# Performance work log

Measured on AMD Instinct MI355X. Metric: run time of the kernel, lower is better.

Reference implementation:

```python
import jax, jax.numpy as jnp
import numpy as np

N = 20000          # nodes
E = 320000         # edges (before self loops)
IN_DIM = 64
HID = 128
HEADS = 4
LAYERS = 3
GRAPHS = 64
NEG_SLOPE = 0.2
LN_EPS = 1e-5


def setup_inputs() -> dict:
    key = jax.random.key(0)
    ks = jax.random.split(key, 12)
    x = jax.random.normal(ks[0], (N, IN_DIM), dtype=jnp.float32)
    edge_index = jax.random.randint(ks[1], (2, E), 0, N, dtype=jnp.int64)
    batch = jnp.sort(jax.random.randint(ks[2], (N,), 0, GRAPHS, dtype=jnp.int64))
    s = 0.05
    W_in = jax.random.normal(ks[3], (IN_DIM, HID), dtype=jnp.float32) * s
    b_in = jnp.zeros((HID,), dtype=jnp.float32)
    Ws = jax.random.normal(ks[4], (LAYERS, HID, HEADS * HID), dtype=jnp.float32) * s
    att_src = jax.random.normal(ks[5], (LAYERS, HEADS, HID), dtype=jnp.float32) * s
    att_dst = jax.random.normal(ks[6], (LAYERS, HEADS, HID), dtype=jnp.float32) * s
    conv_b = jnp.zeros((LAYERS, HID), dtype=jnp.float32)
    ln_g = jnp.ones((LAYERS, HID), dtype=jnp.float32)
    ln_b = jnp.zeros((LAYERS, HID), dtype=jnp.float32)
    return {"x": x, "edge_index": edge_index, "batch": batch,
            "W_in": W_in, "b_in": b_in, "Ws": Ws, "att_src": att_src,
            "att_dst": att_dst, "conv_b": conv_b, "ln_g": ln_g, "ln_b": ln_b}


def _gat_layer(x, src, dst, W, a_src, a_dst, bias):
    # x: [N, HID] -> h: [N, HEADS, HID]
    h = (x @ W).reshape(N, HEADS, HID)
    alpha_s = jnp.einsum('nhc,hc->nh', h, a_src)   # [N, H]
    alpha_d = jnp.einsum('nhc,hc->nh', h, a_dst)   # [N, H]
    e = jax.nn.leaky_relu(alpha_s[src] + alpha_d[dst], NEG_SLOPE)  # [E', H]
    # segment softmax over destination node (every node has a self loop)
    m = jax.ops.segment_max(e, dst, num_segments=N)
    e = jnp.exp(e - m[dst])
    denom = jax.ops.segment_sum(e, dst, num_segments=N)
    a = e / (denom[dst] + 1e-16)                    # [E', H]
    msg = h[src] * a[:, :, None]                    # [E', H, HID]
    out = jax.ops.segment_sum(msg, dst, num_segments=N)  # [N, H, HID]
    return out.mean(axis=1) + bias                  # concat=False -> head mean


def _layer_norm(x, g, b):
    mu = x.mean(axis=-1, keepdims=True)
    var = ((x - mu) ** 2).mean(axis=-1, keepdims=True)
    return (x - mu) * jax.lax.rsqrt(var + LN_EPS) * g + b


def reference(x, edge_index, batch, W_in, b_in, Ws, att_src, att_dst, conv_b, ln_g, ln_b):
    # add self loops (PyG GATConv default)
    loops = jnp.arange(N, dtype=edge_index.dtype)
    src = jnp.concatenate([edge_index[0], loops])
    dst = jnp.concatenate([edge_index[1], loops])

    h = x @ W_in + b_in
    for l in range(LAYERS):
        conv = _gat_layer(h, src, dst, Ws[l], att_src[l], att_dst[l], conv_b[l])
        h = _layer_norm(jax.nn.relu(conv) + h, ln_g[l], ln_b[l])

    # global mean pool over graphs
    sums = jax.ops.segment_sum(h, batch, num_segments=GRAPHS)
    cnt = jax.ops.segment_sum(jnp.ones((N,), dtype=h.dtype), batch, num_segments=GRAPHS)
    return sums / jnp.maximum(cnt, 1.0)[:, None]
```

## Files before the change

kernel.cpp:

```cpp
#include <hip/hip_runtime.h>
#include <hip/hip_bf16.h>
#include <math.h>

#define N_NODES 20000
#define N_EDGES 320000
#define IN_DIM 64
#define HID 128
#define HEADS 4
#define LAYERS 3
#define GRAPHS 64
#define TOT_E (N_EDGES + N_NODES)
#define NEG_SLOPE 0.2f
#define LN_EPS 1e-5f
#define MAXD 96
#define OB 132

typedef __attribute__((ext_vector_type(8))) short short8v;
typedef __attribute__((ext_vector_type(4))) float f32x4;
typedef __attribute__((ext_vector_type(2))) float f32x2;

__device__ __forceinline__ float blo(unsigned int u) { return __uint_as_float(u << 16); }
__device__ __forceinline__ float bhi(unsigned int u) { return __uint_as_float(u & 0xffff0000u); }


__global__ void zero_kernel(int* __restrict__ cursor) {
    int i = blockIdx.x * blockDim.x + threadIdx.x;
    if (i < N_NODES) cursor[i] = 0;
}

__global__ void fill_slots(const int* __restrict__ ei, int* __restrict__ cursor,
                           int* __restrict__ slots) {
    int e = blockIdx.x * blockDim.x + threadIdx.x;
    if (e >= TOT_E) return;
    int src, dst;
    if (e < N_EDGES) { src = ei[e]; dst = ei[N_EDGES + e]; }
    else { src = e - N_EDGES; dst = src; }
    int pos = atomicAdd(&cursor[dst], 1);
    if (pos < MAXD) slots[dst * MAXD + pos] = src;
}


#define NV (LAYERS * 128 * 512)
#define NWIN (HID * IN_DIM)
#define NX (N_NODES * IN_DIM)
#define NU (LAYERS * HEADS * HID)

__global__ void pack_all(const float* __restrict__ Ws, const float* __restrict__ W_in,
                         const float* __restrict__ x, const float* __restrict__ att_src,
                         const float* __restrict__ att_dst,
                         __hip_bfloat16* __restrict__ Vt, __hip_bfloat16* __restrict__ Wt_in,
                         __hip_bfloat16* __restrict__ xb,
                         float* __restrict__ u_s, float* __restrict__ u_d) {
    int i = blockIdx.x * blockDim.x + threadIdx.x;
    if (i < NV) {
        int l = i / 65536;
        int r = i % 65536;
        int c = r / 512, hk = r % 512;
        int hh = hk >> 7, k = hk & 127;
        Vt[i] = __float2bfloat16(0.25f * Ws[(size_t)l * 65536 + k * 512 + hh * 128 + c]);
    } else if (i < NV + NWIN) {
        int r = i - NV;
        int n = r / 64, k = r % 64;
        Wt_in[r] = __float2bfloat16(W_in[k * 128 + n]);
    } else if (i < NV + NWIN + NX) {
        int r = i - NV - NWIN;
        xb[r] = __float2bfloat16(x[r]);
    } else if (i < NV + NWIN + NX + NU) {
        int t = i - NV - NWIN - NX;
        int l = t / 512;
        int r = t % 512;
        int hh = r / 128, k = r % 128;
        const float* wrow = Ws + (size_t)l * 65536 + k * 512 + hh * 128;
        const float* as = att_src + l * 512 + hh * 128;
        const float* ad = att_dst + l * 512 + hh * 128;
        float ss = 0.f, sd = 0.f;
        for (int c = 0; c < 128; ++c) {
            float w = wrow[c];
            ss = fmaf(w, as[c], ss);
            sd = fmaf(w, ad[c], sd);
        }
        u_s[t] = ss; u_d[t] = sd;
    }
}


__global__ __launch_bounds__(256) void gemm_in(
    const __hip_bfloat16* __restrict__ Ax,
    const __hip_bfloat16* __restrict__ Bt,
    const float* __restrict__ bias,
    const float* __restrict__ u_s0, const float* __restrict__ u_d0,
    float* __restrict__ h, unsigned char* __restrict__ h8,
    float* __restrict__ a_s, float* __restrict__ a_d) {
    __shared__ __hip_bfloat16 As[64 * 64];
    const int M_ = N_NODES;
    int tid = threadIdx.x;
    int lane = tid & 63, w = tid >> 6;
    int lr = lane & 15, lg = lane >> 4;
    int row0 = blockIdx.x * 64;
#pragma unroll
    for (int it = 0; it < 2; ++it) {
        int chunk = it * 256 + tid;
        int row = chunk >> 3, c8 = chunk & 7;
        int sc = c8 ^ (row & 7);
        int gr = row0 + row; if (gr >= M_) gr = M_ - 1;
        const __hip_bfloat16* src = Ax + (size_t)gr * 64 + sc * 8;
        __builtin_amdgcn_global_load_lds(
            (const void __attribute__((address_space(1)))*)src,
            (void __attribute__((address_space(3)))*)(As + chunk * 8), 16, 0, 0);
    }
    __syncthreads();

    f32x4 acc[8] = {};
    int rl = w * 16 + lr;
#pragma unroll
    for (int ks = 0; ks < 2; ++ks) {
        int kc = ks * 4 + lg;
        short8v a = *(const short8v*)&As[(rl * 8 + (kc ^ (rl & 7))) * 8];
#pragma unroll
        for (int nf = 0; nf < 8; ++nf) {
            short8v b = *(const short8v*)&Bt[(size_t)(nf * 16 + lr) * 64 + ks * 32 + lg * 8];
            acc[nf] = __builtin_amdgcn_mfma_f32_16x16x32_bf16(a, b, acc[nf], 0, 0, 0);
        }
    }

    float cb[8], us[4][8], ud[4][8];
#pragma unroll
    for (int nf = 0; nf < 8; ++nf) cb[nf] = bias[nf * 16 + lr];
#pragma unroll
    for (int hh = 0; hh < 4; ++hh)
#pragma unroll
        for (int nf = 0; nf < 8; ++nf) {
            us[hh][nf] = u_s0[hh * 128 + nf * 16 + lr];
            ud[hh][nf] = u_d0[hh * 128 + nf * 16 + lr];
        }

#pragma unroll
    for (int j = 0; j < 4; ++j) {
        int r = row0 + w * 16 + lg * 4 + j;
        if (r >= M_) continue;
        float vals[8];
#pragma unroll
        for (int nf = 0; nf < 8; ++nf) {
            float v = acc[nf][j] + cb[nf];
            vals[nf] = v;
            h[(size_t)r * HID + nf * 16 + lr] = v;
            int d = __builtin_amdgcn_cvt_pk_fp8_f32(v, v, 0, false);
            h8[(size_t)r * HID + nf * 16 + lr] = (unsigned char)(d & 0xff);
        }
#pragma unroll
        for (int hh = 0; hh < 4; ++hh) {
            float ps = 0.f, pd = 0.f;
#pragma unroll
            for (int nf = 0; nf < 8; ++nf) {
                ps = fmaf(vals[nf], us[hh][nf], ps);
                pd = fmaf(vals[nf], ud[hh][nf], pd);
            }
            ps += __shfl_xor(ps, 1); pd += __shfl_xor(pd, 1);
            ps += __shfl_xor(ps, 2); pd += __shfl_xor(pd, 2);
            ps += __shfl_xor(ps, 4); pd += __shfl_xor(pd, 4);
            ps += __shfl_xor(ps, 8); pd += __shfl_xor(pd, 8);
            if (lr == 0) { a_s[r * 4 + hh] = ps; a_d[r * 4 + hh] = pd; }
        }
    }
}


__global__ __launch_bounds__(256) void layer_fused(
    const int* __restrict__ deg_arr, const int* __restrict__ slots,
    const unsigned char* __restrict__ h8i, const float* __restrict__ a_si,
    const float* __restrict__ a_di,
    const __hip_bfloat16* __restrict__ Vt,
    const float* __restrict__ conv_b, const float* __restrict__ ln_g,
    const float* __restrict__ ln_b,
    const float* __restrict__ u_sn, const float* __restrict__ u_dn,
    float* __restrict__ h, unsigned char* __restrict__ h8o,
    float* __restrict__ a_so, float* __restrict__ a_do, int last) {
    __shared__ __attribute__((aligned(16))) __hip_bfloat16 aggLds[16 * 512];
    __shared__ __attribute__((aligned(16))) char uMem[16 * OB * 4];
    float* outb = (float*)uMem;
    float (*eLds)[MAXD * 4] = (float(*)[MAXD * 4])uMem;
    int (*sLds)[MAXD] = (int(*)[MAXD])(uMem + 4 * MAXD * 4 * 4);

    int tid = threadIdx.x;
    int lane = tid & 63, wv = tid >> 6;
    int row0 = blockIdx.x * 16;
    int hh = lane >> 4;
    int j  = lane & 15;
    const unsigned char* hbase = h8i + j * 8;

    for (int t = 0; t < 4; ++t) {
        int row = wv * 4 + t;
        int n = row0 + row;
        int deg = deg_arr[n]; if (deg > MAXD) deg = MAXD;
        int beg = n * MAXD;

        int ja = lane >> 2, ha = lane & 3;
        float adh = a_di[n * 4 + ha];
        float mx = -3.4e38f;
        for (int c = 0; c < deg; c += 16) {
            int idx = c + ja;
            float e = -3.4e38f;
            if (idx < deg) {
                int s = slots[beg + idx];
                if (ha == 0) sLds[wv][idx] = s;
                e = a_si[s * 4 + ha] + adh;
                e = (e > 0.f) ? e : NEG_SLOPE * e;
            }
            eLds[wv][idx * 4 + ha] = e;
            mx = fmaxf(mx, e);
        }
        mx = fmaxf(mx, __shfl_xor(mx, 4));
        mx = fmaxf(mx, __shfl_xor(mx, 8));
        mx = fmaxf(mx, __shfl_xor(mx, 16));
        mx = fmaxf(mx, __shfl_xor(mx, 32));
        float dsum = 0.f;
        for (int c = 0; c < deg; c += 16) {
            int idx = c + ja;
            if (idx < deg) {
                float p = __expf(eLds[wv][idx * 4 + ha] - mx);
                eLds[wv][idx * 4 + ha] = p;
                dsum += p;
            }
        }
        dsum += __shfl_xor(dsum, 4);
        dsum += __shfl_xor(dsum, 8);
        dsum += __shfl_xor(dsum, 16);
        dsum += __shfl_xor(dsum, 32);
        float dh = __shfl(dsum, hh);
        float inv_own = 1.f / (dh + 1e-16f);

        float acc[8] = {0.f, 0.f, 0.f, 0.f, 0.f, 0.f, 0.f, 0.f};
        int i = 0;
        for (; i + 3 < deg; i += 4) {
            int ss[4]; float pp[4]; uint2 uu[4];
#pragma unroll
            for (int k = 0; k < 4; ++k) {
                ss[k] = sLds[wv][i + k];
                pp[k] = eLds[wv][(i + k) * 4 + hh];
            }
#pragma unroll
            for (int k = 0; k < 4; ++k)
                uu[k] = *(const uint2*)(hbase + (size_t)ss[k] * HID);
#pragma unroll
            for (int k = 0; k < 4; ++k) {
                f32x2 a01 = __builtin_amdgcn_cvt_pk_f32_fp8(uu[k].x, false);
                f32x2 a23 = __builtin_amdgcn_cvt_pk_f32_fp8(uu[k].x, true);
                f32x2 a45 = __builtin_amdgcn_cvt_pk_f32_fp8(uu[k].y, false);
                f32x2 a67 = __builtin_amdgcn_cvt_pk_f32_fp8(uu[k].y, true);
                acc[0] = fmaf(pp[k], a01[0], acc[0]);
                acc[1] = fmaf(pp[k], a01[1], acc[1]);
                acc[2] = fmaf(pp[k], a23[0], acc[2]);
                acc[3] = fmaf(pp[k], a23[1], acc[3]);
                acc[4] = fmaf(pp[k], a45[0], acc[4]);
                acc[5] = fmaf(pp[k], a45[1], acc[5]);
                acc[6] = fmaf(pp[k], a67[0], acc[6]);
                acc[7] = fmaf(pp[k], a67[1], acc[7]);
            }
        }
        for (; i < deg; ++i) {
            int s0 = sLds[wv][i];
            float p0 = eLds[wv][i * 4 + hh];
            uint2 u0 = *(const uint2*)(hbase + (size_t)s0 * HID);
            f32x2 a01 = __builtin_amdgcn_cvt_pk_f32_fp8(u0.x, false);
            f32x2 a23 = __builtin_amdgcn_cvt_pk_f32_fp8(u0.x, true);
            f32x2 a45 = __builtin_amdgcn_cvt_pk_f32_fp8(u0.y, false);
            f32x2 a67 = __builtin_amdgcn_cvt_pk_f32_fp8(u0.y, true);
            acc[0] = fmaf(p0, a01[0], acc[0]);
            acc[1] = fmaf(p0, a01[1], acc[1]);
            acc[2] = fmaf(p0, a23[0], acc[2]);
            acc[3] = fmaf(p0, a23[1], acc[3]);
            acc[4] = fmaf(p0, a45[0], acc[4]);
            acc[5] = fmaf(p0, a45[1], acc[5]);
            acc[6] = fmaf(p0, a67[0], acc[6]);
            acc[7] = fmaf(p0, a67[1], acc[7]);
        }

        __hip_bfloat162 q[4];
#pragma unroll
        for (int k = 0; k < 4; ++k) {
            q[k].x = __float2bfloat16(acc[2 * k] * inv_own);
            q[k].y = __float2bfloat16(acc[2 * k + 1] * inv_own);
        }
        *(uint4*)&aggLds[row * 512 + (16 * hh + (j ^ row)) * 8] = *(uint4*)q;
    }
    __syncthreads();

    int lr = lane & 15, lg = lane >> 4;
    f32x4 macc[2] = {};
    const __hip_bfloat16* Bb0 = Vt + (size_t)(wv * 32 + lr) * 512;
    const __hip_bfloat16* Bb1 = Vt + (size_t)(wv * 32 + 16 + lr) * 512;
#pragma unroll
    for (int ks = 0; ks < 16; ++ks) {
        int kc = ks * 4 + lg;
        int pos = (kc & ~15) | ((kc & 15) ^ lr);
        short8v a = *(const short8v*)&aggLds[lr * 512 + pos * 8];
        int ko = ks * 32 + lg * 8;
        short8v b0 = *(const short8v*)(Bb0 + ko);
        short8v b1 = *(const short8v*)(Bb1 + ko);
        macc[0] = __builtin_amdgcn_mfma_f32_16x16x32_bf16(a, b0, macc[0], 0, 0, 0);
        macc[1] = __builtin_amdgcn_mfma_f32_16x16x32_bf16(a, b1, macc[1], 0, 0, 0);
    }
    __syncthreads();
#pragma unroll
    for (int nf = 0; nf < 2; ++nf)
#pragma unroll
        for (int jj = 0; jj < 4; ++jj)
            outb[(lg * 4 + jj) * OB + wv * 32 + nf * 16 + lr] = macc[nf][jj];
    __syncthreads();

    int row = tid >> 4, q = tid & 15;
    int r = row0 + row;
    int c0 = q * 8;
    float v[8];
#pragma unroll
    for (int c = 0; c < 8; ++c) v[c] = outb[row * OB + c0 + c];

    float4 cb0 = *(const float4*)&conv_b[c0];
    float4 cb1 = *(const float4*)&conv_b[c0 + 4];
    float cb[8] = {cb0.x, cb0.y, cb0.z, cb0.w, cb1.x, cb1.y, cb1.z, cb1.w};
    float4 h0 = *(const float4*)&h[(size_t)r * HID + c0];
    float4 h1 = *(const float4*)&h[(size_t)r * HID + c0 + 4];
    float hr[8] = {h0.x, h0.y, h0.z, h0.w, h1.x, h1.y, h1.z, h1.w};
    float s1 = 0.f;
#pragma unroll
    for (int c = 0; c < 8; ++c) {
        v[c] = fmaxf(v[c] + cb[c], 0.f) + hr[c];
        s1 += v[c];
    }
    s1 += __shfl_xor(s1, 1); s1 += __shfl_xor(s1, 2);
    s1 += __shfl_xor(s1, 4); s1 += __shfl_xor(s1, 8);
    float mu = s1 * (1.f / HID);
    float s2 = 0.f;
#pragma unroll
    for (int c = 0; c < 8; ++c) {
        v[c] -= mu;
        s2 += v[c] * v[c];
    }
    s2 += __shfl_xor(s2, 1); s2 += __shfl_xor(s2, 2);
    s2 += __shfl_xor(s2, 4); s2 += __shfl_xor(s2, 8);
    float rstd = rsqrtf(s2 * (1.f / HID) + LN_EPS);
    float4 g0 = *(const float4*)&ln_g[c0];
    float4 g1 = *(const float4*)&ln_g[c0 + 4];
    float4 b0 = *(const float4*)&ln_b[c0];
    float4 b1 = *(const float4*)&ln_b[c0 + 4];
    float gg[8] = {g0.x, g0.y, g0.z, g0.w, g1.x, g1.y, g1.z, g1.w};
    float bb[8] = {b0.x, b0.y, b0.z, b0.w, b1.x, b1.y, b1.z, b1.w};
    float o[8];
#pragma unroll
    for (int c = 0; c < 8; ++c) o[c] = v[c] * rstd * gg[c] + bb[c];

    *(float4*)&h[(size_t)r * HID + c0] = make_float4(o[0], o[1], o[2], o[3]);
    *(float4*)&h[(size_t)r * HID + c0 + 4] = make_float4(o[4], o[5], o[6], o[7]);
    int d0 = 0, d1 = 0;
    d0 = __builtin_amdgcn_cvt_pk_fp8_f32(o[0], o[1], d0, false);
    d0 = __builtin_amdgcn_cvt_pk_fp8_f32(o[2], o[3], d0, true);
    d1 = __builtin_amdgcn_cvt_pk_fp8_f32(o[4], o[5], d1, false);
    d1 = __builtin_amdgcn_cvt_pk_fp8_f32(o[6], o[7], d1, true);
    *(uint2*)&h8o[(size_t)r * HID + c0] = make_uint2((unsigned)d0, (unsigned)d1);

    if (!last) {
#pragma unroll
        for (int ah = 0; ah < 4; ++ah) {
            float4 usa = *(const float4*)&u_sn[ah * 128 + c0];
            float4 usb = *(const float4*)&u_sn[ah * 128 + c0 + 4];
            float4 uda = *(const float4*)&u_dn[ah * 128 + c0];
            float4 udb = *(const float4*)&u_dn[ah * 128 + c0 + 4];
            float ps = o[0] * usa.x + o[1] * usa.y + o[2] * usa.z + o[3] * usa.w +
                       o[4] * usb.x + o[5] * usb.y + o[6] * usb.z + o[7] * usb.w;
            float pd = o[0] * uda.x + o[1] * uda.y + o[2] * uda.z + o[3] * uda.w +
                       o[4] * udb.x + o[5] * udb.y + o[6] * udb.z + o[7] * udb.w;
            ps += __shfl_xor(ps, 1); pd += __shfl_xor(pd, 1);
            ps += __shfl_xor(ps, 2); pd += __shfl_xor(pd, 2);
            ps += __shfl_xor(ps, 4); pd += __shfl_xor(pd, 4);
            ps += __shfl_xor(ps, 8); pd += __shfl_xor(pd, 8);
            if (q == 0) { a_so[r * 4 + ah] = ps; a_do[r * 4 + ah] = pd; }
        }
    }
}


__global__ __launch_bounds__(128) void pool2_kernel(
    const float* __restrict__ h, const int* __restrict__ batch,
    float* __restrict__ out) {
    int g = blockIdx.x;
    int c = threadIdx.x;
    __shared__ int sLo, sHi;
    if (c == 0) {
        int lo = 0, hi = N_NODES;
        while (lo < hi) { int m = (lo + hi) >> 1; if (batch[m] < g) lo = m + 1; else hi = m; }
        sLo = lo;
        hi = N_NODES;
        while (lo < hi) { int m = (lo + hi) >> 1; if (batch[m] < g + 1) lo = m + 1; else hi = m; }
        sHi = lo;
    }
    __syncthreads();
    int lo = sLo, hi = sHi;
    float s0 = 0.f, s1 = 0.f, s2 = 0.f, s3 = 0.f;
    int n = lo;
    for (; n + 3 < hi; n += 4) {
        s0 += h[(size_t)n * HID + c];
        s1 += h[(size_t)(n + 1) * HID + c];
        s2 += h[(size_t)(n + 2) * HID + c];
        s3 += h[(size_t)(n + 3) * HID + c];
    }
    for (; n < hi; ++n) s0 += h[(size_t)n * HID + c];
    float s = (s0 + s1) + (s2 + s3);
    int cnt = hi - lo; if (cnt < 1) cnt = 1;
    out[g * HID + c] = s / (float)cnt;
}


extern "C" void kernel_launch(void* const* d_in, const int* in_sizes, int n_in,
                              void* d_out, int out_size, void* d_ws, size_t ws_size,
                              hipStream_t stream) {
    const float* x      = (const float*)d_in[0];
    const int*   ei     = (const int*)d_in[1];
    const int*   batch  = (const int*)d_in[2];
    const float* W_in   = (const float*)d_in[3];
    const float* b_in   = (const float*)d_in[4];
    const float* Ws     = (const float*)d_in[5];
    const float* att_src= (const float*)d_in[6];
    const float* att_dst= (const float*)d_in[7];
    const float* conv_b = (const float*)d_in[8];
    const float* ln_g   = (const float*)d_in[9];
    const float* ln_b   = (const float*)d_in[10];
    float* out = (float*)d_out;

    char* ws = (char*)d_ws;
    size_t off = 0;
    auto alloc = [&](size_t bytes) -> void* {
        void* p = ws + off;
        off = (off + bytes + 255) & ~(size_t)255;
        return p;
    };
    float* h            = (float*)alloc((size_t)N_NODES * HID * 4);
    unsigned char* h8a  = (unsigned char*)alloc((size_t)N_NODES * HID);
    unsigned char* h8b  = (unsigned char*)alloc((size_t)N_NODES * HID);
    __hip_bfloat16* Vt  = (__hip_bfloat16*)alloc((size_t)NV * 2);
    __hip_bfloat16* Wti = (__hip_bfloat16*)alloc((size_t)NWIN * 2);
    __hip_bfloat16* xb  = (__hip_bfloat16*)alloc((size_t)NX * 2);
    float* u_s    = (float*)alloc((size_t)NU * 4);
    float* u_d    = (float*)alloc((size_t)NU * 4);
    float* a_sa   = (float*)alloc((size_t)N_NODES * HEADS * 4);
    float* a_sb   = (float*)alloc((size_t)N_NODES * HEADS * 4);
    float* a_da   = (float*)alloc((size_t)N_NODES * HEADS * 4);
    float* a_db   = (float*)alloc((size_t)N_NODES * HEADS * 4);
    int* cursor   = (int*)alloc(N_NODES * 4);
    int* slots    = (int*)alloc((size_t)N_NODES * MAXD * 4);

    zero_kernel<<<(N_NODES + 255) / 256, 256, 0, stream>>>(cursor);
    fill_slots<<<(TOT_E + 255) / 256, 256, 0, stream>>>(ei, cursor, slots);
    pack_all<<<(NV + NWIN + NX + NU + 255) / 256, 256, 0, stream>>>(
        Ws, W_in, x, att_src, att_dst, Vt, Wti, xb, u_s, u_d);

    gemm_in<<<(N_NODES + 63) / 64, 256, 0, stream>>>(
        xb, Wti, b_in, u_s, u_d, h, h8a, a_sa, a_da);

    unsigned char* h8bufs[2] = {h8a, h8b};
    float* asbufs[2] = {a_sa, a_sb};
    float* adbufs[2] = {a_da, a_db};
    for (int l = 0; l < LAYERS; ++l) {
        int cur = l & 1, nxt = (l + 1) & 1;
        int lu = (l + 1 < LAYERS) ? l + 1 : l;
        layer_fused<<<N_NODES / 16, 256, 0, stream>>>(
            cursor, slots, h8bufs[cur], asbufs[cur], adbufs[cur],
            Vt + (size_t)l * 65536,
            conv_b + (size_t)l * HID, ln_g + (size_t)l * HID, ln_b + (size_t)l * HID,
            u_s + (size_t)lu * 512, u_d + (size_t)lu * 512,
            h, h8bufs[nxt], asbufs[nxt], adbufs[nxt], (l == LAYERS - 1) ? 1 : 0);
    }

    pool2_kernel<<<GRAPHS, 128, 0, stream>>>(h, batch, out);
}
```

Baseline: 213.7 us.

## Double layer_fused block to 512 threads with two rows per wave

```diff
diff --git a/kernel.cpp b/kernel.cpp
--- a/kernel.cpp
+++ b/kernel.cpp
@@ -165,7 +165,7 @@
 }
 
 
-__global__ __launch_bounds__(256) void layer_fused(
+__global__ __launch_bounds__(512, 8) void layer_fused(
     const int* __restrict__ deg_arr, const int* __restrict__ slots,
     const unsigned char* __restrict__ h8i, const float* __restrict__ a_si,
     const float* __restrict__ a_di,
@@ -176,10 +176,10 @@
     float* __restrict__ h, unsigned char* __restrict__ h8o,
     float* __restrict__ a_so, float* __restrict__ a_do, int last) {
     __shared__ __attribute__((aligned(16))) __hip_bfloat16 aggLds[16 * 512];
-    __shared__ __attribute__((aligned(16))) char uMem[16 * OB * 4];
+    __shared__ __attribute__((aligned(16))) char uMem[15360];
     float* outb = (float*)uMem;
     float (*eLds)[MAXD * 4] = (float(*)[MAXD * 4])uMem;
-    int (*sLds)[MAXD] = (int(*)[MAXD])(uMem + 4 * MAXD * 4 * 4);
+    int (*sLds)[MAXD] = (int(*)[MAXD])(uMem + 8 * MAXD * 4 * 4);
 
     int tid = threadIdx.x;
     int lane = tid & 63, wv = tid >> 6;
@@ -188,8 +188,8 @@
     int j  = lane & 15;
     const unsigned char* hbase = h8i + j * 8;
 
-    for (int t = 0; t < 4; ++t) {
-        int row = wv * 4 + t;
+    for (int t = 0; t < 2; ++t) {
+        int row = wv * 2 + t;
         int n = row0 + row;
         int deg = deg_arr[n]; if (deg > MAXD) deg = MAXD;
         int beg = n * MAXD;
@@ -286,93 +286,78 @@
     __syncthreads();
 
     int lr = lane & 15, lg = lane >> 4;
-    f32x4 macc[2] = {};
-    const __hip_bfloat16* Bb0 = Vt + (size_t)(wv * 32 + lr) * 512;
-    const __hip_bfloat16* Bb1 = Vt + (size_t)(wv * 32 + 16 + lr) * 512;
+    f32x4 macc = {};
+    const __hip_bfloat16* Bb = Vt + (size_t)(wv * 16 + lr) * 512;
 #pragma unroll
     for (int ks = 0; ks < 16; ++ks) {
         int kc = ks * 4 + lg;
         int pos = (kc & ~15) | ((kc & 15) ^ lr);
         short8v a = *(const short8v*)&aggLds[lr * 512 + pos * 8];
-        int ko = ks * 32 + lg * 8;
-        short8v b0 = *(const short8v*)(Bb0 + ko);
-        short8v b1 = *(const short8v*)(Bb1 + ko);
-        macc[0] = __builtin_amdgcn_mfma_f32_16x16x32_bf16(a, b0, macc[0], 0, 0, 0);
-        macc[1] = __builtin_amdgcn_mfma_f32_16x16x32_bf16(a, b1, macc[1], 0, 0, 0);
-    }
+        short8v b = *(const short8v*)(Bb + ks * 32 + lg * 8);
+        macc = __builtin_amdgcn_mfma_f32_16x16x32_bf16(a, b, macc, 0, 0, 0);
+    }
+#pragma unroll
+    for (int jj = 0; jj < 4; ++jj)
+        outb[(lg * 4 + jj) * OB + wv * 16 + lr] = macc[jj];
     __syncthreads();
-#pragma unroll
-    for (int nf = 0; nf < 2; ++nf)
-#pragma unroll
-        for (int jj = 0; jj < 4; ++jj)
-            outb[(lg * 4 + jj) * OB + wv * 32 + nf * 16 + lr] = macc[nf][jj];
-    __syncthreads();
-
-    int row = tid >> 4, q = tid & 15;
+
+    int row = tid >> 5, q = tid & 31;
     int r = row0 + row;
-    int c0 = q * 8;
-    float v[8];
-#pragma unroll
-    for (int c = 0; c < 8; ++c) v[c] = outb[row * OB + c0 + c];
-
-    float4 cb0 = *(const float4*)&conv_b[c0];
-    float4 cb1 = *(const float4*)&conv_b[c0 + 4];
-    float cb[8] = {cb0.x, cb0.y, cb0.z, cb0.w, cb1.x, cb1.y, cb1.z, cb1.w};
-    float4 h0 = *(const float4*)&h[(size_t)r * HID + c0];
-    float4 h1 = *(const float4*)&h[(size_t)r * HID + c0 + 4];
-    float hr[8] = {h0.x, h0.y, h0.z, h0.w, h1.x, h1.y, h1.z, h1.w};
+    int c0 = q * 4;
+    float v[4];
+#pragma unroll
+    for (int c = 0; c < 4; ++c) v[c] = outb[row * OB + c0 + c];
+
+    float4 cbv = *(const float4*)&conv_b[c0];
+    float cb[4] = {cbv.x, cbv.y, cbv.z, cbv.w};
+    float4 hv = *(const float4*)&h[(size_t)r * HID + c0];
+    float hr[4] = {hv.x, hv.y, hv.z, hv.w};
     float s1 = 0.f;
 #pragma unroll
-    for (int c = 0; c < 8; ++c) {
+    for (int c = 0; c < 4; ++c) {
         v[c] = fmaxf(v[c] + cb[c], 0.f) + hr[c];
         s1 += v[c];
     }
     s1 += __shfl_xor(s1, 1); s1 += __shfl_xor(s1, 2);
     s1 += __shfl_xor(s1, 4); s1 += __shfl_xor(s1, 8);
+    s1 += __shfl_xor(s1, 16);
     float mu = s1 * (1.f / HID);
     float s2 = 0.f;
 #pragma unroll
-    for (int c = 0; c < 8; ++c) {
+    for (int c = 0; c < 4; ++c) {
         v[c] -= mu;
         s2 += v[c] * v[c];
     }
     s2 += __shfl_xor(s2, 1); s2 += __shfl_xor(s2, 2);
     s2 += __shfl_xor(s2, 4); s2 += __shfl_xor(s2, 8);
+    s2 += __shfl_xor(s2, 16);
     float rstd = rsqrtf(s2 * (1.f / HID) + LN_EPS);
-    float4 g0 = *(const float4*)&ln_g[c0];
-    float4 g1 = *(const float4*)&ln_g[c0 + 4];
-    float4 b0 = *(const float4*)&ln_b[c0];
-    float4 b1 = *(const float4*)&ln_b[c0 + 4];
-    float gg[8] = {g0.x, g0.y, g0.z, g0.w, g1.x, g1.y, g1.z, g1.w};
-    float bb[8] = {b0.x, b0.y, b0.z, b0.w, b1.x, b1.y, b1.z, b1.w};
-    float o[8];
-#pragma unroll
-    for (int c = 0; c < 8; ++c) o[c] = v[c] * rstd * gg[c] + bb[c];
+    float4 gv = *(const float4*)&ln_g[c0];
+    float4 bv = *(const float4*)&ln_b[c0];
+    float gg[4] = {gv.x, gv.y, gv.z, gv.w};
+    float bb[4] = {bv.x, bv.y, bv.z, bv.w};
+    float o[4];
+#pragma unroll
+    for (int c = 0; c < 4; ++c) o[c] = v[c] * rstd * gg[c] + bb[c];
 
     *(float4*)&h[(size_t)r * HID + c0] = make_float4(o[0], o[1], o[2], o[3]);
-    *(float4*)&h[(size_t)r * HID + c0 + 4] = make_float4(o[4], o[5], o[6], o[7]);
-    int d0 = 0, d1 = 0;
+    int d0 = 0;
     d0 = __builtin_amdgcn_cvt_pk_fp8_f32(o[0], o[1], d0, false);
     d0 = __builtin_amdgcn_cvt_pk_fp8_f32(o[2], o[3], d0, true);
-    d1 = __builtin_amdgcn_cvt_pk_fp8_f32(o[4], o[5], d1, false);
-    d1 = __builtin_amdgcn_cvt_pk_fp8_f32(o[6], o[7], d1, true);
-    *(uint2*)&h8o[(size_t)r * HID + c0] = make_uint2((unsigned)d0, (unsigned)d1);
+    *(unsigned int*)&h8o[(size_t)r * HID + c0] = (unsigned int)d0;
 
     if (!last) {
 #pragma unroll
         for (int ah = 0; ah < 4; ++ah) {
-            float4 usa = *(const float4*)&u_sn[ah * 128 + c0];
-            float4 usb = *(const float4*)&u_sn[ah * 128 + c0 + 4];
-            float4 uda = *(const float4*)&u_dn[ah * 128 + c0];
-            float4 udb = *(const float4*)&u_dn[ah * 128 + c0 + 4];
-            float ps = o[0] * usa.x + o[1] * usa.y + o[2] * usa.z + o[3] * usa.w +
-                       o[4] * usb.x + o[5] * usb.y + o[6] * usb.z + o[7] * usb.w;
-            float pd = o[0] * uda.x + o[1] * uda.y + o[2] * uda.z + o[3] * uda.w +
-                       o[4] * udb.x + o[5] * udb.y + o[6] * udb.z + o[7] * udb.w;
+            float4 usv = *(const float4*)&u_sn[ah * 128 + c0];
+            float4 udv = *(const float4*)&u_dn[ah * 128 + c0];
+            float ps = o[0] * usv.x + o[1] * usv.y + o[2] * usv.z + o[3] * usv.w;
+            float pd = o[0] * udv.x + o[1] * udv.y + o[2] * udv.z + o[3] * udv.w;
             ps += __shfl_xor(ps, 1); pd += __shfl_xor(pd, 1);
             ps += __shfl_xor(ps, 2); pd += __shfl_xor(pd, 2);
             ps += __shfl_xor(ps, 4); pd += __shfl_xor(pd, 4);
             ps += __shfl_xor(ps, 8); pd += __shfl_xor(pd, 8);
+            ps += __shfl_xor(ps, 16); pd += __shfl_xor(pd, 16);
             if (q == 0) { a_so[r * 4 + ah] = ps; a_do[r * 4 + ah] = pd; }
         }
     }
@@ -462,7 +447,7 @@
     for (int l = 0; l < LAYERS; ++l) {
         int cur = l & 1, nxt = (l + 1) & 1;
         int lu = (l + 1 < LAYERS) ? l + 1 : l;
-        layer_fused<<<N_NODES / 16, 256, 0, stream>>>(
+        layer_fused<<<N_NODES / 16, 512, 0, stream>>>(
             cursor, slots, h8bufs[cur], asbufs[cur], adbufs[cur],
             Vt + (size_t)l * 65536,
             conv_b + (size_t)l * HID, ln_g + (size_t)l * HID, ln_b + (size_t)l * HID,
```

Result: slower. 226.1 us (+5.8%).
